# Performance work log

Measured on AMD Instinct MI355X. Metric: run time of the kernel, lower is better.

The kernel has to match this reference:

```python
import jax, jax.numpy as jnp
import numpy as np

B, N, E = 64, 2048, 32768
F_IN, NHID, RULES = 256, 512, 128
RATIO = 0.5
K1 = int(np.ceil(RATIO * N)); K2 = int(np.ceil(RATIO * K1)); K3 = int(np.ceil(RATIO * K2))


def _gcn(x, src, dst, em, W, b):
    # GCNConv with self-loops and symmetric normalization; em is a float edge-validity mask.
    n = x.shape[0]
    h = x @ W  # [n, out]
    deg = jax.ops.segment_sum(em, dst, num_segments=n) + 1.0  # in-degree + self-loop
    dinv = jax.lax.rsqrt(deg)
    coef = dinv[src] * dinv[dst] * em  # [E]
    agg = jax.ops.segment_sum(h[src] * coef[:, None], dst, num_segments=n)
    return agg + h / deg[:, None] + b  # second term = self-loop with norm 1/deg


def _sag_pool(x, src, dst, em, Wg, bg, k):
    # SAGPooling: GCN scorer, per-graph top-k, scale kept nodes by tanh(score), filter+reindex edges.
    n = x.shape[0]
    score = _gcn(x, src, dst, em, Wg, bg)[:, 0]  # [n]
    vals, perm = jax.lax.top_k(score, k)
    xk = x[perm] * jnp.tanh(vals)[:, None]  # [k, F]
    newidx = jnp.full((n,), -1, dtype=src.dtype).at[perm].set(jnp.arange(k, dtype=src.dtype))
    ns, nd = newidx[src], newidx[dst]
    keep = em * (ns >= 0).astype(em.dtype) * (nd >= 0).astype(em.dtype)
    return xk, jnp.maximum(ns, 0), jnp.maximum(nd, 0), keep


_gcn_b = jax.vmap(_gcn, in_axes=(0, 0, 0, 0, None, None))
_pool_b = jax.vmap(_sag_pool, in_axes=(0, 0, 0, 0, None, None, None))


def setup_inputs() -> dict:
    key = jax.random.key(0)
    ks = jax.random.split(key, 16)
    def w(k, shape, fan_in):
        return jax.random.normal(k, shape, jnp.float32) * (1.0 / np.sqrt(fan_in))
    return {
        "x": jax.random.normal(ks[0], (B, N, F_IN), jnp.float32),
        "src": jax.random.randint(ks[1], (B, E), 0, N, jnp.int32),
        "dst": jax.random.randint(ks[2], (B, E), 0, N, jnp.int32),
        "W1": w(ks[3], (F_IN, NHID), F_IN), "b1": jnp.zeros((NHID,), jnp.float32),
        "Wp1": w(ks[4], (NHID, 1), NHID), "bp1": jnp.zeros((1,), jnp.float32),
        "W2": w(ks[5], (NHID, NHID), NHID), "b2": jnp.zeros((NHID,), jnp.float32),
        "Wp2": w(ks[6], (NHID, 1), NHID), "bp2": jnp.zeros((1,), jnp.float32),
        "W3": w(ks[7], (NHID, NHID), NHID), "b3": jnp.zeros((NHID,), jnp.float32),
        "Wp3": w(ks[8], (NHID, 1), NHID), "bp3": jnp.zeros((1,), jnp.float32),
        "lin1_W": w(ks[9], (2 * NHID, NHID), 2 * NHID), "lin1_b": jnp.zeros((NHID,), jnp.float32),
        "lin2_W": w(ks[10], (NHID, NHID // 2), NHID), "lin2_b": jnp.zeros((NHID // 2,), jnp.float32),
        "pi_W": w(ks[11], (NHID // 2, RULES), NHID // 2), "pi_b": jnp.zeros((RULES,), jnp.float32),
        "v_W": w(ks[12], (NHID // 2, 1), NHID // 2), "v_b": jnp.zeros((1,), jnp.float32),
    }


def reference(x, src, dst, W1, b1, Wp1, bp1, W2, b2, Wp2, bp2, W3, b3, Wp3, bp3,
              lin1_W, lin1_b, lin2_W, lin2_b, pi_W, pi_b, v_W, v_b):
    em = jnp.ones(src.shape, x.dtype)
    h = jax.nn.relu(_gcn_b(x, src, dst, em, W1, b1))
    h, s, d, em = _pool_b(h, src, dst, em, Wp1, bp1, K1)
    x1 = jnp.concatenate([h.max(axis=1), h.mean(axis=1)], axis=1)  # [B, 2*NHID]
    h = jax.nn.relu(_gcn_b(h, s, d, em, W2, b2))
    h, s, d, em = _pool_b(h, s, d, em, Wp2, bp2, K2)
    x2 = jnp.concatenate([h.max(axis=1), h.mean(axis=1)], axis=1)
    h = jax.nn.relu(_gcn_b(h, s, d, em, W3, b3))
    h, s, d, em = _pool_b(h, s, d, em, Wp3, bp3, K3)
    x3 = jnp.concatenate([h.max(axis=1), h.mean(axis=1)], axis=1)
    z = x1 + x2 + x3
    z = jax.nn.relu(z @ lin1_W + lin1_b)
    z = jax.nn.relu(z @ lin2_W + lin2_b)
    pi = jax.nn.log_softmax(z @ pi_W + pi_b, axis=1)
    v = jax.nn.relu(z @ v_W + v_b)
    return pi, v
```

## Files before the change

kernel.cpp:

```cpp
#include <hip/hip_runtime.h>
#include <math.h>
#include <cstdint>

#define B_   64
#define N_   2048
#define E_   32768
#define FIN  256
#define H_   512

typedef __bf16 bf16x8 __attribute__((ext_vector_type(8)));
typedef float  f32x4  __attribute__((ext_vector_type(4)));

__device__ __forceinline__ unsigned short f2bf(float f) {
  unsigned u = __float_as_uint(f);
  u += 0x7FFF + ((u >> 16) & 1);
  return (unsigned short)(u >> 16);
}
__device__ __forceinline__ unsigned pk2(float a, float b) {
  return (unsigned)f2bf(a) | ((unsigned)f2bf(b) << 16);
}
__device__ __forceinline__ float bflo(unsigned u) { return __uint_as_float(u << 16); }
__device__ __forceinline__ float bfhi(unsigned u) { return __uint_as_float(u & 0xFFFF0000u); }

__device__ __forceinline__ void accum8(float* acc, uint4 u, float c) {
  acc[0] += c * bflo(u.x); acc[1] += c * bfhi(u.x);
  acc[2] += c * bflo(u.y); acc[3] += c * bfhi(u.y);
  acc[4] += c * bflo(u.z); acc[5] += c * bfhi(u.z);
  acc[6] += c * bflo(u.w); acc[7] += c * bfhi(u.w);
}

__device__ __forceinline__ void glds16(const void* g, void* l) {
  __builtin_amdgcn_global_load_lds(
      (const __attribute__((address_space(1))) unsigned int*)g,
      (__attribute__((address_space(3))) unsigned int*)l, 16, 0, 0);
}

__global__ void xcvt_k(const float* __restrict__ x, unsigned short* __restrict__ xb) {
  int i = blockIdx.x * 256 + threadIdx.x;
  float4 f = reinterpret_cast<const float4*>(x)[i];
  uint2 o; o.x = pk2(f.x, f.y); o.y = pk2(f.z, f.w);
  reinterpret_cast<uint2*>(xb)[i] = o;
}

__global__ void wcvt_k(const float* __restrict__ W, unsigned short* __restrict__ Wt, int K) {
  int idx = blockIdx.x * 256 + threadIdx.x;
  int k = idx >> 9, n = idx & 511;
  Wt[n * K + k] = f2bf(W[idx]);
}

__global__ __launch_bounds__(256) void gemm_mfma(
    const unsigned short* __restrict__ Xb,
    const int* __restrict__ perm, const float* __restrict__ tanhv,
    const unsigned short* __restrict__ Wt, unsigned short* __restrict__ Y,
    int K, int kl2, int nsl2,
    const float* __restrict__ bias, const float* __restrict__ wp, float* __restrict__ hs) {
  __shared__ __align__(16) char smem[34816];
  const int tid = threadIdx.x;
  const int w = tid >> 6, L = tid & 63;
  const int bid = blockIdx.x;
  const int xcd = bid & 7;
  const int t = bid >> 3;
  const int colb = t & 3;
  const int strip = ((t >> 2) << 3) + xcd;
  const int m0 = strip * 128;
  const int n0 = colb * 128;
  const int e = L & 15, q = L >> 4;

  const int sw3 = (L >> 3) & 7;
  const int cA = (w * 64 + L) ^ sw3;
  const int rloc = cA >> 2;
  const int kcs = (cA & 3) * 8;

  f32x4 acc[4][4];
#pragma unroll
  for (int j = 0; j < 4; j++)
#pragma unroll
    for (int nn = 0; nn < 4; nn++) acc[j][nn] = (f32x4){0.f, 0.f, 0.f, 0.f};

  size_t asrc[2];
#pragma unroll
  for (int i = 0; i < 2; i++) {
    int g = m0 + i * 64 + rloc;
    size_t row;
    if (perm) {
      int b = g >> kl2;
      int node = perm[g];
      row = (size_t)(b << nsl2) + node;
    } else {
      row = (size_t)g;
    }
    asrc[i] = row * (size_t)K + kcs;
  }
  size_t bsrc[2];
#pragma unroll
  for (int i = 0; i < 2; i++) bsrc[i] = (size_t)(n0 + i * 64 + rloc) * K + kcs;

  const int fo = e * 4 + q;
  const int fosw = fo ^ (fo >> 3);
  const int lofs = w * 64 * 16;

  const int nk = K >> 5;
  {
    char* Ab = smem;
    char* Bb = smem + 16384;
    glds16(Xb + asrc[0], Ab + 0 * 4096 + lofs);
    glds16(Xb + asrc[1], Ab + 1 * 4096 + lofs);
    glds16(Wt + bsrc[0], Bb + 0 * 4096 + lofs);
    glds16(Wt + bsrc[1], Bb + 1 * 4096 + lofs);
  }
  __syncthreads();
  int cur = 0;
  for (int kt = 0; kt < nk; ++kt) {
    if (kt + 1 < nk) {
      const int k0 = (kt + 1) << 5;
      char* Ab = smem + (cur ^ 1) * 8192;
      char* Bb = smem + 16384 + (cur ^ 1) * 8192;
      glds16(Xb + asrc[0] + k0, Ab + 0 * 4096 + lofs);
      glds16(Xb + asrc[1] + k0, Ab + 1 * 4096 + lofs);
      glds16(Wt + bsrc[0] + k0, Bb + 0 * 4096 + lofs);
      glds16(Wt + bsrc[1] + k0, Bb + 1 * 4096 + lofs);
    }
    const uint4* As = (const uint4*)(smem + cur * 8192);
    const uint4* Bs = (const uint4*)(smem + 16384 + cur * 8192);
    bf16x8 af[4], bfr[4];
#pragma unroll
    for (int j = 0; j < 4; j++) af[j]  = __builtin_bit_cast(bf16x8, As[((w & 1) * 4 + j) * 64 + fosw]);
#pragma unroll
    for (int j = 0; j < 4; j++) bfr[j] = __builtin_bit_cast(bf16x8, Bs[((w >> 1) * 4 + j) * 64 + fosw]);
#pragma unroll
    for (int j = 0; j < 4; j++)
#pragma unroll
      for (int nn = 0; nn < 4; nn++)
        acc[j][nn] = __builtin_amdgcn_mfma_f32_16x16x32_bf16(af[j], bfr[nn], acc[j][nn], 0, 0, 0);
    __syncthreads();
    cur ^= 1;
  }

  const int RS = 136;
  unsigned short* Csm = (unsigned short*)smem;
  float bs[4], wsv[4];
#pragma unroll
  for (int nn = 0; nn < 4; nn++) {
    int coly = n0 + ((w >> 1) * 4 + nn) * 16 + e;
    bs[nn]  = bias ? bias[coly] : 0.f;
    wsv[nn] = wp ? wp[coly] : 0.f;
  }
#pragma unroll
  for (int j = 0; j < 4; j++) {
    int mt = (w & 1) * 4 + j;
#pragma unroll
    for (int r = 0; r < 4; r++) {
      int lrow = mt * 16 + q * 4 + r;
      int grow = m0 + lrow;
      float t2 = tanhv ? tanhv[grow] : 1.0f;
      float p = 0.f;
#pragma unroll
      for (int nn = 0; nn < 4; nn++) {
        int lcol = (w >> 1) * 64 + nn * 16 + e;
        float v = acc[j][nn][r] * t2;
        if (bias) v = fmaxf(v + bs[nn], 0.f);
        Csm[lrow * RS + lcol] = f2bf(v);
        p += v * wsv[nn];
      }
      if (wp) {
        p += __shfl_xor(p, 1, 64); p += __shfl_xor(p, 2, 64);
        p += __shfl_xor(p, 4, 64); p += __shfl_xor(p, 8, 64);
        if ((L & 15) == 0) atomicAdd(&hs[grow], p);
      }
    }
  }
  __syncthreads();
  const int rbase = tid >> 4, ci = tid & 15;
#pragma unroll
  for (int pass = 0; pass < 8; ++pass) {
    int lrow = pass * 16 + rbase;
    uint4 u = *(const uint4*)(Csm + lrow * RS + ci * 8);
    *(uint4*)(Y + (size_t)(m0 + lrow) * 512 + n0 + ci * 8) = u;
  }
}

template <int NL2, bool REINDEX>
__global__ __launch_bounds__(512) void csr_k(
    const int* __restrict__ srcO, const int* __restrict__ dstO,
    const int* __restrict__ newidx,
    int* __restrict__ srcN, int* __restrict__ dstN,
    int* __restrict__ rowptr, float* __restrict__ deg, float* __restrict__ dinv,
    int* __restrict__ col, float* __restrict__ ce) {
  const int n = 1 << NL2;
  const int b = blockIdx.x, tid = threadIdx.x;
  __shared__ int   lcnt[1 << NL2];
  __shared__ int   ch[512];
  __shared__ float ldv[1 << NL2];
  __shared__ int   lnew[REINDEX ? (2 << NL2) : 1];
  const int eb = b << 15;

  for (int i = tid; i < n; i += 512) lcnt[i] = 0;
  if (REINDEX)
    for (int i = tid; i < 2 * n; i += 512) lnew[i] = newidx[(b << (NL2 + 1)) + i];
  __syncthreads();

  if (REINDEX) {
    for (int e2 = tid; e2 < E_; e2 += 512) {
      int dd = dstO[eb + e2];
      int sN = 0, dN = -1;
      if (dd >= 0) {
        int ss = srcO[eb + e2];
        int ns = lnew[ss], nd = lnew[dd];
        if (ns >= 0 && nd >= 0) { sN = ns; dN = nd; atomicAdd(&lcnt[nd], 1); }
      }
      srcN[eb + e2] = sN; dstN[eb + e2] = dN;
    }
  } else {
    for (int e2 = tid; e2 < E_; e2 += 512) {
      int d = dstO[eb + e2];
      if (d >= 0) atomicAdd(&lcnt[d], 1);
    }
  }
  __syncthreads();

  const int per = n >> 9;
  const int base = tid * per;
  int lc[per];
  int s = 0;
#pragma unroll
  for (int i = 0; i < per; i++) { lc[i] = lcnt[base + i]; s += lc[i]; }
  ch[tid] = s;
  __syncthreads();
  for (int off = 1; off < 512; off <<= 1) {
    int v = (tid >= off) ? ch[tid - off] : 0;
    __syncthreads();
    ch[tid] += v;
    __syncthreads();
  }
  int run = (tid == 0) ? 0 : ch[tid - 1];
#pragma unroll
  for (int i = 0; i < per; i++) {
    int v = lc[i];
    int g = base + i;
    rowptr[b * (n + 1) + g] = run;
    lcnt[g] = run;
    float d = (float)(v + 1);
    deg[(b << NL2) + g] = d;
    float iv = 1.0f / sqrtf(d);
    ldv[g] = iv;
    dinv[(b << NL2) + g] = iv;
    run += v;
  }
  if (tid == 511) rowptr[b * (n + 1) + n] = run;
  __syncthreads();

  const int* S2 = REINDEX ? srcN : srcO;
  const int* D2 = REINDEX ? dstN : dstO;
  for (int e2 = tid; e2 < E_; e2 += 512) {
    int d = D2[eb + e2];
    if (d >= 0) {
      int ss = S2[eb + e2];
      int pos = atomicAdd(&lcnt[d], 1);
      col[eb + pos] = ss;
      ce[eb + pos] = ldv[ss] * ldv[d];
    }
  }
}

__global__ __launch_bounds__(256) void aggx_k(
    const unsigned short* __restrict__ X,
    const int* __restrict__ rowptr, const int* __restrict__ col,
    const float* __restrict__ ce, const float* __restrict__ deg,
    unsigned short* __restrict__ Xa) {
  const int hw = threadIdx.x >> 5, hl = threadIdx.x & 31;
  const int xcd = blockIdx.x & 7;
  const int slot = blockIdx.x >> 3;
  const int gslot = slot >> 8;
  const int v8 = slot & 255;
  const int b = (gslot << 3) + xcd;
  const int v = v8 * 8 + hw;
  const int bbase = b << 11;
  const int vg = bbase + v;
  const int rb = b * (N_ + 1) + v;
  const int st = rowptr[rb], en = rowptr[rb + 1];
  const int* cb = col + (b << 15);
  const float* cee = ce + (b << 15);
  const unsigned short* Xb_ = X + (size_t)bbase * 256 + hl * 8;
  float acc[8] = {0.f, 0.f, 0.f, 0.f, 0.f, 0.f, 0.f, 0.f};
  int e2 = st;
  for (; e2 + 4 <= en; e2 += 4) {
    int s0 = cb[e2], s1 = cb[e2 + 1], s2 = cb[e2 + 2], s3 = cb[e2 + 3];
    float c0 = cee[e2], c1 = cee[e2 + 1], c2 = cee[e2 + 2], c3 = cee[e2 + 3];
    uint4 u0 = *(const uint4*)(Xb_ + (size_t)s0 * 256);
    uint4 u1 = *(const uint4*)(Xb_ + (size_t)s1 * 256);
    uint4 u2 = *(const uint4*)(Xb_ + (size_t)s2 * 256);
    uint4 u3 = *(const uint4*)(Xb_ + (size_t)s3 * 256);
    accum8(acc, u0, c0); accum8(acc, u1, c1);
    accum8(acc, u2, c2); accum8(acc, u3, c3);
  }
  for (; e2 < en; e2++) {
    uint4 u = *(const uint4*)(Xb_ + (size_t)cb[e2] * 256);
    accum8(acc, u, cee[e2]);
  }
  {
    uint4 u = *(const uint4*)(Xb_ + (size_t)v * 256);
    accum8(acc, u, 1.0f / deg[vg]);
  }
  uint4 o;
  o.x = pk2(acc[0], acc[1]); o.y = pk2(acc[2], acc[3]);
  o.z = pk2(acc[4], acc[5]); o.w = pk2(acc[6], acc[7]);
  *(uint4*)(Xa + (size_t)vg * 256 + hl * 8) = o;
}

template <int NL2>
__global__ __launch_bounds__(256) void agg_k(
    const unsigned short* __restrict__ H,
    const int* __restrict__ rowptr, const int* __restrict__ col,
    const float* __restrict__ ce, const float* __restrict__ deg,
    const float* __restrict__ bias, const float* __restrict__ wp,
    unsigned short* __restrict__ C, float* __restrict__ hs) {
  const int n = 1 << NL2;
  const int xcd = blockIdx.x & 7;
  const int slot = blockIdx.x >> 3;
  const int gslot = slot >> (NL2 - 2);
  const int v4 = slot & ((1 << (NL2 - 2)) - 1);
  const int b = (gslot << 3) + xcd;
  const int w = threadIdx.x >> 6, L = threadIdx.x & 63;
  const int v = v4 * 4 + w;
  const int bbase = b << NL2;
  const int vg = bbase + v;
  const int rb = b * (n + 1) + v;
  const int st = rowptr[rb], en = rowptr[rb + 1];
  const int* cb = col + (b << 15);
  const float* cee = ce + (b << 15);
  const unsigned short* Hb_ = H + (size_t)bbase * 512 + (size_t)L * 8;

  float acc[8] = {0.f, 0.f, 0.f, 0.f, 0.f, 0.f, 0.f, 0.f};
  int e2 = st;
  for (; e2 + 4 <= en; e2 += 4) {
    int s0 = cb[e2], s1 = cb[e2 + 1], s2 = cb[e2 + 2], s3 = cb[e2 + 3];
    float c0 = cee[e2], c1 = cee[e2 + 1], c2 = cee[e2 + 2], c3 = cee[e2 + 3];
    uint4 u0 = *(const uint4*)(Hb_ + (size_t)s0 * 512);
    uint4 u1 = *(const uint4*)(Hb_ + (size_t)s1 * 512);
    uint4 u2 = *(const uint4*)(Hb_ + (size_t)s2 * 512);
    uint4 u3 = *(const uint4*)(Hb_ + (size_t)s3 * 512);
    accum8(acc, u0, c0); accum8(acc, u1, c1);
    accum8(acc, u2, c2); accum8(acc, u3, c3);
  }
  for (; e2 < en; e2++) {
    int s = cb[e2];
    uint4 u = *(const uint4*)(Hb_ + (size_t)s * 512);
    accum8(acc, u, cee[e2]);
  }
  {
    float idg = 1.0f / deg[vg];
    uint4 u = *(const uint4*)(Hb_ + (size_t)v * 512);
    accum8(acc, u, idg);
  }
  float4 bLo = *(const float4*)(bias + L * 8);
  float4 bHi = *(const float4*)(bias + L * 8 + 4);
  acc[0] = fmaxf(acc[0] + bLo.x, 0.f); acc[1] = fmaxf(acc[1] + bLo.y, 0.f);
  acc[2] = fmaxf(acc[2] + bLo.z, 0.f); acc[3] = fmaxf(acc[3] + bLo.w, 0.f);
  acc[4] = fmaxf(acc[4] + bHi.x, 0.f); acc[5] = fmaxf(acc[5] + bHi.y, 0.f);
  acc[6] = fmaxf(acc[6] + bHi.z, 0.f); acc[7] = fmaxf(acc[7] + bHi.w, 0.f);
  uint4 o;
  o.x = pk2(acc[0], acc[1]); o.y = pk2(acc[2], acc[3]);
  o.z = pk2(acc[4], acc[5]); o.w = pk2(acc[6], acc[7]);
  *(uint4*)(C + (size_t)vg * 512 + L * 8) = o;
  float4 wLo = *(const float4*)(wp + L * 8);
  float4 wHi = *(const float4*)(wp + L * 8 + 4);
  float p = acc[0] * wLo.x + acc[1] * wLo.y + acc[2] * wLo.z + acc[3] * wLo.w
          + acc[4] * wHi.x + acc[5] * wHi.y + acc[6] * wHi.z + acc[7] * wHi.w;
#pragma unroll
  for (int off = 32; off > 0; off >>= 1) p += __shfl_down(p, off, 64);
  if (L == 0) hs[vg] = p;
}

__global__ void scoreagg_k(const float* __restrict__ hs, const int* __restrict__ rowptr,
                           const int* __restrict__ col, const float* __restrict__ ce,
                           const float* __restrict__ deg, const float* __restrict__ bp,
                           float* __restrict__ score, int nl2) {
  int idx = blockIdx.x * 256 + threadIdx.x;
  int n = 1 << nl2;
  int b = idx >> nl2, v = idx & (n - 1);
  int rb = b * (n + 1) + v;
  int st = rowptr[rb], en = rowptr[rb + 1];
  const int* cb = col + (b << 15);
  const float* cee = ce + (b << 15);
  int bbase = b << nl2;
  float acc = 0.f;
  int e = st;
  for (; e + 4 <= en; e += 4) {
    acc += hs[bbase + cb[e]] * cee[e] + hs[bbase + cb[e + 1]] * cee[e + 1]
         + hs[bbase + cb[e + 2]] * cee[e + 2] + hs[bbase + cb[e + 3]] * cee[e + 3];
  }
  for (; e < en; e++) acc += hs[bbase + cb[e]] * cee[e];
  score[idx] = acc + hs[idx] / deg[idx] + bp[0];
}

__global__ __launch_bounds__(1024) void topk_k(const float* __restrict__ score, int* __restrict__ perm,
                                               float* __restrict__ tanhv, int* __restrict__ newidx,
                                               int n, int k) {
  int b = blockIdx.x, tid = threadIdx.x;
  __shared__ float ss[2048];
  __shared__ int si[2048];
  for (int i = tid; i < n; i += 1024) { ss[i] = score[b * n + i]; si[i] = i; }
  __syncthreads();
  for (int size = 2; size <= n; size <<= 1) {
    for (int stride = size >> 1; stride > 0; stride >>= 1) {
      for (int i = tid; i < n; i += 1024) {
        int j = i ^ stride;
        if (j > i) {
          bool up = ((i & size) == 0);
          float fi = ss[i], fj = ss[j];
          int ii = si[i], ij = si[j];
          bool iBefore = (fi > fj) || (fi == fj && ii < ij);
          bool sw = up ? (!iBefore) : iBefore;
          if (sw) { ss[i] = fj; ss[j] = fi; si[i] = ij; si[j] = ii; }
        }
      }
      __syncthreads();
    }
  }
  for (int r = tid; r < n; r += 1024) newidx[b * n + si[r]] = (r < k) ? r : -1;
  for (int r = tid; r < k; r += 1024) { perm[b * k + r] = si[r]; tanhv[b * k + r] = tanhf(ss[r]); }
}

__global__ __launch_bounds__(512) void statsp_k(const unsigned short* __restrict__ C,
    const int* __restrict__ perm, const float* __restrict__ tv,
    float* __restrict__ zp, int nsl2, int k, int kch) {
  int b = blockIdx.x, rg = blockIdx.y, f = threadIdx.x;
  int r0 = rg * kch;
  float mx = -1e30f, sm = 0.f;
#pragma unroll 4
  for (int r = r0; r < r0 + kch; r++) {
    int node = perm[b * k + r];
    float t = tv[b * k + r];
    float val = __uint_as_float((unsigned)C[((size_t)((b << nsl2) + node)) * 512 + f] << 16) * t;
    mx = fmaxf(mx, val); sm += val;
  }
  zp[(size_t)(b * 8 + rg) * 1024 + f] = mx;
  zp[(size_t)(b * 8 + rg) * 1024 + 512 + f] = sm;
}

__global__ __launch_bounds__(512) void statsr_k(const float* __restrict__ zp,
                                                float* __restrict__ z, int k) {
  int b = blockIdx.x, f = threadIdx.x;
  float mx = -1e30f, sm = 0.f;
#pragma unroll
  for (int g = 0; g < 8; g++) {
    mx = fmaxf(mx, zp[(size_t)(b * 8 + g) * 1024 + f]);
    sm += zp[(size_t)(b * 8 + g) * 1024 + 512 + f];
  }
  z[b * 1024 + f] += mx;
  z[b * 1024 + 512 + f] += sm / (float)k;
}

__global__ __launch_bounds__(256) void mlp1_k(const float* __restrict__ z,
                                              const float* __restrict__ W1,
                                              float* __restrict__ zp1) {
  const int kc = blockIdx.x & 7;
  const int b = blockIdx.x >> 3;
  const int tid = threadIdx.x;
  __shared__ float zs[128];
  if (tid < 128) zs[tid] = z[b * 1024 + kc * 128 + tid];
  __syncthreads();
  float a0 = 0.f, a1 = 0.f;
  const float* Wb = W1 + (size_t)(kc * 128) * 512 + tid * 2;
#pragma unroll 4
  for (int i = 0; i < 128; i++) {
    float2 w = *(const float2*)(Wb + (size_t)i * 512);
    float zi = zs[i];
    a0 += zi * w.x; a1 += zi * w.y;
  }
  reinterpret_cast<float2*>(zp1 + ((size_t)(kc * 64 + b)) * 512)[tid] = make_float2(a0, a1);
}

__global__ __launch_bounds__(256) void mlp2_k(const float* __restrict__ zp1,
                                              const float* __restrict__ b1,
                                              const float* __restrict__ W2,
                                              float* __restrict__ zp2) {
  const int kc = blockIdx.x & 1;
  const int b = blockIdx.x >> 1;
  const int tid = threadIdx.x;
  __shared__ float z1s[256];
  {
    int i = kc * 256 + tid;
    float a = b1[i];
#pragma unroll
    for (int g = 0; g < 8; g++) a += zp1[((size_t)(g * 64 + b)) * 512 + i];
    z1s[tid] = fmaxf(a, 0.f);
  }
  __syncthreads();
  float a = 0.f;
  const float* Wb = W2 + (size_t)(kc * 256) * 256 + tid;
#pragma unroll 4
  for (int i = 0; i < 256; i++) a += z1s[i] * Wb[(size_t)i * 256];
  zp2[((size_t)(kc * 64 + b)) * 256 + tid] = a;
}

__global__ __launch_bounds__(128) void mlp3_k(const float* __restrict__ zp2,
                                              const float* __restrict__ b2,
                                              const float* __restrict__ piW,
                                              const float* __restrict__ pib,
                                              const float* __restrict__ vW,
                                              const float* __restrict__ vb,
                                              float* __restrict__ out) {
  const int b = blockIdx.x, tid = threadIdx.x;
  __shared__ float z2s[256];
  __shared__ float wred[4];
  __shared__ float sred[2];
  for (int t = tid; t < 256; t += 128) {
    float a = b2[t] + zp2[(size_t)b * 256 + t] + zp2[(size_t)(64 + b) * 256 + t];
    z2s[t] = fmaxf(a, 0.f);
  }
  __syncthreads();
  float a = pib[tid];
#pragma unroll 4
  for (int i = 0; i < 256; i++) a += z2s[i] * piW[(size_t)i * 128 + tid];
  float vp = z2s[tid] * vW[tid] + z2s[tid + 128] * vW[tid + 128];
  float m = a;
#pragma unroll
  for (int off = 32; off > 0; off >>= 1) {
    vp += __shfl_xor(vp, off, 64);
    m = fmaxf(m, __shfl_xor(m, off, 64));
  }
  const int wv = tid >> 6;
  if ((tid & 63) == 0) { wred[wv] = m; wred[2 + wv] = vp; }
  __syncthreads();
  m = fmaxf(wred[0], wred[1]);
  float s = expf(a - m);
#pragma unroll
  for (int off = 32; off > 0; off >>= 1) s += __shfl_xor(s, off, 64);
  if ((tid & 63) == 0) sred[wv] = s;
  __syncthreads();
  s = sred[0] + sred[1];
  if (tid == 0) out[B_ * 128 + b] = fmaxf(vb[0] + wred[2] + wred[3], 0.f);
  out[b * 128 + tid] = a - m - logf(s);
}

extern "C" void kernel_launch(void* const* d_in, const int* in_sizes, int n_in,
                              void* d_out, int out_size, void* d_ws, size_t ws_size,
                              hipStream_t stream) {
  const float* x    = (const float*)d_in[0];
  const int*   src0 = (const int*)d_in[1];
  const int*   dst0 = (const int*)d_in[2];
  const float* W1   = (const float*)d_in[3];
  const float* b1   = (const float*)d_in[4];
  const float* Wp1  = (const float*)d_in[5];
  const float* bp1  = (const float*)d_in[6];
  const float* W2   = (const float*)d_in[7];
  const float* b2   = (const float*)d_in[8];
  const float* Wp2  = (const float*)d_in[9];
  const float* bp2  = (const float*)d_in[10];
  const float* W3   = (const float*)d_in[11];
  const float* b3   = (const float*)d_in[12];
  const float* Wp3  = (const float*)d_in[13];
  const float* bp3  = (const float*)d_in[14];
  const float* l1W  = (const float*)d_in[15];
  const float* l1b  = (const float*)d_in[16];
  const float* l2W  = (const float*)d_in[17];
  const float* l2b  = (const float*)d_in[18];
  const float* piW  = (const float*)d_in[19];
  const float* pib  = (const float*)d_in[20];
  const float* vW   = (const float*)d_in[21];
  const float* vb   = (const float*)d_in[22];
  float* out = (float*)d_out;
  (void)in_sizes; (void)n_in; (void)out_size; (void)ws_size;

  unsigned short* Cb = (unsigned short*)d_in[0];

  char* base = (char*)d_ws;
  size_t off = 0;
  auto alloc = [&](size_t bytes) -> void* {
    void* r = base + off;
    off += (bytes + 255) & ~(size_t)255;
    return r;
  };
  unsigned short* Hb   = (unsigned short*)alloc((size_t)B_ * 1024 * H_ * 2);
  unsigned short* xb   = (unsigned short*)alloc((size_t)B_ * N_ * FIN * 2);
  unsigned short* Xa   = (unsigned short*)alloc((size_t)B_ * N_ * FIN * 2);
  unsigned short* W1t  = (unsigned short*)alloc((size_t)512 * 256 * 2);
  unsigned short* W2t  = (unsigned short*)alloc((size_t)512 * 512 * 2);
  unsigned short* W3t  = (unsigned short*)alloc((size_t)512 * 512 * 2);
  int*   srcA   = (int*)alloc((size_t)B_ * E_ * 4);
  int*   dstA   = (int*)alloc((size_t)B_ * E_ * 4);
  int*   col    = (int*)alloc((size_t)B_ * E_ * 4);
  float* coefE  = (float*)alloc((size_t)B_ * E_ * 4);
  int*   rowptr = (int*)alloc((size_t)B_ * (N_ + 1) * 4);
  float* deg    = (float*)alloc((size_t)B_ * N_ * 4);
  float* dinv   = (float*)alloc((size_t)B_ * N_ * 4);
  float* hs     = (float*)alloc((size_t)B_ * N_ * 4);
  float* score  = (float*)alloc((size_t)B_ * N_ * 4);
  int*   newidx = (int*)alloc((size_t)B_ * N_ * 4);
  int*   perm   = (int*)alloc((size_t)B_ * 1024 * 4);
  float* tanhv  = (float*)alloc((size_t)B_ * 1024 * 4);
  float* zpart  = (float*)alloc((size_t)B_ * 8 * 1024 * 4);
  float* z      = (float*)alloc((size_t)B_ * 1024 * 4);

  float* zp1 = zpart;
  float* zp2 = zpart + (size_t)8 * 64 * 512;

  xcvt_k<<<B_ * N_ * FIN / 4 / 256, 256, 0, stream>>>(x, xb);
  wcvt_k<<<256 * 512 / 256, 256, 0, stream>>>(W1, W1t, 256);
  wcvt_k<<<512 * 512 / 256, 256, 0, stream>>>(W2, W2t, 512);
  wcvt_k<<<512 * 512 / 256, 256, 0, stream>>>(W3, W3t, 512);
  hipMemsetAsync(z, 0, (size_t)B_ * 1024 * 4, stream);

  {
    csr_k<11, false><<<B_, 512, 0, stream>>>(src0, dst0, nullptr, nullptr, nullptr,
                                             rowptr, deg, dinv, col, coefE);
    aggx_k<<<B_ * 2048 / 8, 256, 0, stream>>>(xb, rowptr, col, coefE, deg, Xa);
    hipMemsetAsync(hs, 0, (size_t)B_ * 2048 * 4, stream);
    gemm_mfma<<<B_ * 2048 / 128 * 4, 256, 0, stream>>>(
        Xa, nullptr, nullptr, W1t, Cb, 256, 0, 0, b1, Wp1, hs);
    scoreagg_k<<<B_ * 2048 / 256, 256, 0, stream>>>(hs, rowptr, col, coefE, deg, bp1, score, 11);
    topk_k<<<B_, 1024, 0, stream>>>(score, perm, tanhv, newidx, 2048, 1024);
    statsp_k<<<dim3(B_, 8), 512, 0, stream>>>(Cb, perm, tanhv, zpart, 11, 1024, 128);
    statsr_k<<<B_, 512, 0, stream>>>(zpart, z, 1024);
    csr_k<10, true><<<B_, 512, 0, stream>>>(src0, dst0, newidx, srcA, dstA,
                                            rowptr, deg, dinv, col, coefE);
  }
  {
    gemm_mfma<<<B_ * 1024 / 128 * 4, 256, 0, stream>>>(
        Cb, perm, tanhv, W2t, Hb, 512, 10, 11, nullptr, nullptr, nullptr);
    agg_k<10><<<B_ * 1024 / 4, 256, 0, stream>>>(Hb, rowptr, col, coefE, deg, b2, Wp2, Cb, hs);
    scoreagg_k<<<B_ * 1024 / 256, 256, 0, stream>>>(hs, rowptr, col, coefE, deg, bp2, score, 10);
    topk_k<<<B_, 1024, 0, stream>>>(score, perm, tanhv, newidx, 1024, 512);
    statsp_k<<<dim3(B_, 8), 512, 0, stream>>>(Cb, perm, tanhv, zpart, 10, 512, 64);
    statsr_k<<<B_, 512, 0, stream>>>(zpart, z, 512);
    csr_k<9, true><<<B_, 512, 0, stream>>>(srcA, dstA, newidx, srcA, dstA,
                                           rowptr, deg, dinv, col, coefE);
  }
  {
    gemm_mfma<<<B_ * 512 / 128 * 4, 256, 0, stream>>>(
        Cb, perm, tanhv, W3t, Hb, 512, 9, 10, nullptr, nullptr, nullptr);
    agg_k<9><<<B_ * 512 / 4, 256, 0, stream>>>(Hb, rowptr, col, coefE, deg, b3, Wp3, Cb, hs);
    scoreagg_k<<<B_ * 512 / 256, 256, 0, stream>>>(hs, rowptr, col, coefE, deg, bp3, score, 9);
    topk_k<<<B_, 1024, 0, stream>>>(score, perm, tanhv, newidx, 512, 256);
    statsp_k<<<dim3(B_, 8), 512, 0, stream>>>(Cb, perm, tanhv, zpart, 9, 256, 32);
    statsr_k<<<B_, 512, 0, stream>>>(zpart, z, 256);
  }

  mlp1_k<<<B_ * 8, 256, 0, stream>>>(z, l1W, zp1);
  mlp2_k<<<B_ * 2, 256, 0, stream>>>(zp1, l1b, l2W, zp2);
  mlp3_k<<<B_, 128, 0, stream>>>(zp2, l2b, piW, pib, vW, vb, out);
}
```

Before: 1.123 ms.

## Rebuild CSR via composed node maps and LDS-staged chunked scatter

```diff
diff --git a/kernel.cpp b/kernel.cpp
--- a/kernel.cpp
+++ b/kernel.cpp
@@ -179,86 +179,141 @@
   }
 }
 
-template <int NL2, bool REINDEX>
-__global__ __launch_bounds__(512) void csr_k(
-    const int* __restrict__ srcO, const int* __restrict__ dstO,
-    const int* __restrict__ newidx,
-    int* __restrict__ srcN, int* __restrict__ dstN,
-    int* __restrict__ rowptr, float* __restrict__ deg, float* __restrict__ dinv,
+template <int NL2, int LEVEL>
+__global__ __launch_bounds__(1024) void csr_k(
+    const int* __restrict__ src0, const int* __restrict__ dst0,
+    const int* __restrict__ curNew, int* __restrict__ cmapG,
+    int* __restrict__ rowptr, float* __restrict__ deg,
     int* __restrict__ col, float* __restrict__ ce) {
   const int n = 1 << NL2;
+  const int CAP = 8192;
   const int b = blockIdx.x, tid = threadIdx.x;
-  __shared__ int   lcnt[1 << NL2];
-  __shared__ int   ch[512];
+  __shared__ int   lrp[(1 << NL2) + 1];
+  __shared__ int   cur[1 << NL2];
   __shared__ float ldv[1 << NL2];
-  __shared__ int   lnew[REINDEX ? (2 << NL2) : 1];
+  __shared__ int   ch[1024];
+  __shared__ int   cmap[(LEVEL > 0) ? 2048 : 1];
+  __shared__ int   scol[CAP];
+  __shared__ float sce[CAP];
+  __shared__ int   sr1;
   const int eb = b << 15;
 
-  for (int i = tid; i < n; i += 512) lcnt[i] = 0;
-  if (REINDEX)
-    for (int i = tid; i < 2 * n; i += 512) lnew[i] = newidx[(b << (NL2 + 1)) + i];
-  __syncthreads();
-
-  if (REINDEX) {
-    for (int e2 = tid; e2 < E_; e2 += 512) {
-      int dd = dstO[eb + e2];
-      int sN = 0, dN = -1;
-      if (dd >= 0) {
-        int ss = srcO[eb + e2];
-        int ns = lnew[ss], nd = lnew[dd];
-        if (ns >= 0 && nd >= 0) { sN = ns; dN = nd; atomicAdd(&lcnt[nd], 1); }
+  for (int i = tid; i < n; i += 1024) cur[i] = 0;
+  if (LEVEL == 1) {
+    for (int v = tid; v < 2048; v += 1024) {
+      int m = curNew[(b << 11) + v];
+      cmap[v] = m;
+      cmapG[(b << 11) + v] = m;
+    }
+  } else if (LEVEL == 2) {
+    for (int v = tid; v < 2048; v += 1024) {
+      int p = cmapG[(b << 11) + v];
+      cmap[v] = (p >= 0) ? curNew[(b << 10) + p] : -1;
+    }
+  }
+  __syncthreads();
+
+  for (int e = tid; e < E_; e += 4096) {
+#pragma unroll
+    for (int u = 0; u < 4; u++) {
+      int ei = eb + e + u * 1024;
+      int dd = dst0[ei];
+      if (LEVEL == 0) {
+        atomicAdd(&cur[dd], 1);
+      } else {
+        int md = cmap[dd], ms = cmap[src0[ei]];
+        if (ms >= 0 && md >= 0) atomicAdd(&cur[md], 1);
       }
-      srcN[eb + e2] = sN; dstN[eb + e2] = dN;
-    }
-  } else {
-    for (int e2 = tid; e2 < E_; e2 += 512) {
-      int d = dstO[eb + e2];
-      if (d >= 0) atomicAdd(&lcnt[d], 1);
-    }
-  }
-  __syncthreads();
-
-  const int per = n >> 9;
-  const int base = tid * per;
+    }
+  }
+  __syncthreads();
+
+  const int nth = (n < 1024) ? n : 1024;
+  const int per = (n + 1023) >> 10;
   int lc[per];
   int s = 0;
-#pragma unroll
-  for (int i = 0; i < per; i++) { lc[i] = lcnt[base + i]; s += lc[i]; }
+  if (tid < nth) {
+    int base = tid * per;
+#pragma unroll
+    for (int i = 0; i < per; i++) { lc[i] = cur[base + i]; s += lc[i]; }
+  }
   ch[tid] = s;
   __syncthreads();
-  for (int off = 1; off < 512; off <<= 1) {
-    int v = (tid >= off) ? ch[tid - off] : 0;
+  for (int off2 = 1; off2 < nth; off2 <<= 1) {
+    int v = (tid >= off2) ? ch[tid - off2] : 0;
     __syncthreads();
     ch[tid] += v;
     __syncthreads();
   }
-  int run = (tid == 0) ? 0 : ch[tid - 1];
-#pragma unroll
-  for (int i = 0; i < per; i++) {
-    int v = lc[i];
-    int g = base + i;
-    rowptr[b * (n + 1) + g] = run;
-    lcnt[g] = run;
-    float d = (float)(v + 1);
-    deg[(b << NL2) + g] = d;
-    float iv = 1.0f / sqrtf(d);
-    ldv[g] = iv;
-    dinv[(b << NL2) + g] = iv;
-    run += v;
-  }
-  if (tid == 511) rowptr[b * (n + 1) + n] = run;
-  __syncthreads();
-
-  const int* S2 = REINDEX ? srcN : srcO;
-  const int* D2 = REINDEX ? dstN : dstO;
-  for (int e2 = tid; e2 < E_; e2 += 512) {
-    int d = D2[eb + e2];
-    if (d >= 0) {
-      int ss = S2[eb + e2];
-      int pos = atomicAdd(&lcnt[d], 1);
-      col[eb + pos] = ss;
-      ce[eb + pos] = ldv[ss] * ldv[d];
-    }
+  if (tid < nth) {
+    int run = (tid == 0) ? 0 : ch[tid - 1];
+    int base = tid * per;
+#pragma unroll
+    for (int i = 0; i < per; i++) {
+      int g = base + i;
+      lrp[g] = run;
+      rowptr[b * (n + 1) + g] = run;
+      cur[g] = run;
+      float dd = (float)(lc[i] + 1);
+      deg[(b << NL2) + g] = dd;
+      ldv[g] = 1.0f / sqrtf(dd);
+      run += lc[i];
+    }
+    if (tid == nth - 1) { lrp[n] = run; rowptr[b * (n + 1) + n] = run; }
+  }
+  __syncthreads();
+
+  int r0 = 0;
+  while (r0 < n) {
+    int base0 = lrp[r0];
+    if (tid == 0) sr1 = n + 1;
+    __syncthreads();
+    for (int r = r0 + 1 + tid; r <= n; r += 1024) {
+      if (lrp[r] - base0 > CAP) { atomicMin(&sr1, r); break; }
+    }
+    __syncthreads();
+    int r1 = sr1 - 1;
+    if (r1 > n) r1 = n;
+    if (r1 <= r0) {
+      for (int e = tid; e < E_; e += 1024) {
+        int ei = eb + e;
+        int ss = src0[ei], dd = dst0[ei];
+        int ms, md;
+        if (LEVEL == 0) { ms = ss; md = dd; }
+        else { ms = cmap[ss]; md = cmap[dd]; }
+        if (ms >= 0 && md == r0) {
+          int pos = atomicAdd(&cur[r0], 1);
+          col[eb + pos] = ms;
+          ce[eb + pos] = ldv[ms] * ldv[r0];
+        }
+      }
+      __syncthreads();
+      r0 = r0 + 1;
+      continue;
+    }
+    for (int e = tid; e < E_; e += 4096) {
+#pragma unroll
+      for (int u = 0; u < 4; u++) {
+        int ei = eb + e + u * 1024;
+        int ss = src0[ei], dd = dst0[ei];
+        int ms, md;
+        if (LEVEL == 0) { ms = ss; md = dd; }
+        else { ms = cmap[ss]; md = cmap[dd]; }
+        if (ms >= 0 && md >= r0 && md < r1) {
+          int pos = atomicAdd(&cur[md], 1);
+          scol[pos - base0] = ms;
+          sce[pos - base0] = ldv[ms] * ldv[md];
+        }
+      }
+    }
+    __syncthreads();
+    int cnt = lrp[r1] - base0;
+    for (int i = tid; i < cnt; i += 1024) {
+      col[eb + base0 + i] = scol[i];
+      ce[eb + base0 + i] = sce[i];
+    }
+    __syncthreads();
+    r0 = r1;
   }
 }
 
@@ -578,13 +633,11 @@
   unsigned short* W1t  = (unsigned short*)alloc((size_t)512 * 256 * 2);
   unsigned short* W2t  = (unsigned short*)alloc((size_t)512 * 512 * 2);
   unsigned short* W3t  = (unsigned short*)alloc((size_t)512 * 512 * 2);
-  int*   srcA   = (int*)alloc((size_t)B_ * E_ * 4);
-  int*   dstA   = (int*)alloc((size_t)B_ * E_ * 4);
   int*   col    = (int*)alloc((size_t)B_ * E_ * 4);
   float* coefE  = (float*)alloc((size_t)B_ * E_ * 4);
+  int*   cmapG  = (int*)alloc((size_t)B_ * N_ * 4);
   int*   rowptr = (int*)alloc((size_t)B_ * (N_ + 1) * 4);
   float* deg    = (float*)alloc((size_t)B_ * N_ * 4);
-  float* dinv   = (float*)alloc((size_t)B_ * N_ * 4);
   float* hs     = (float*)alloc((size_t)B_ * N_ * 4);
   float* score  = (float*)alloc((size_t)B_ * N_ * 4);
   int*   newidx = (int*)alloc((size_t)B_ * N_ * 4);
@@ -603,8 +656,8 @@
   hipMemsetAsync(z, 0, (size_t)B_ * 1024 * 4, stream);
 
   {
-    csr_k<11, false><<<B_, 512, 0, stream>>>(src0, dst0, nullptr, nullptr, nullptr,
-                                             rowptr, deg, dinv, col, coefE);
+    csr_k<11, 0><<<B_, 1024, 0, stream>>>(src0, dst0, nullptr, nullptr,
+                                          rowptr, deg, col, coefE);
     aggx_k<<<B_ * 2048 / 8, 256, 0, stream>>>(xb, rowptr, col, coefE, deg, Xa);
     hipMemsetAsync(hs, 0, (size_t)B_ * 2048 * 4, stream);
     gemm_mfma<<<B_ * 2048 / 128 * 4, 256, 0, stream>>>(
@@ -613,8 +666,8 @@
     topk_k<<<B_, 1024, 0, stream>>>(score, perm, tanhv, newidx, 2048, 1024);
     statsp_k<<<dim3(B_, 8), 512, 0, stream>>>(Cb, perm, tanhv, zpart, 11, 1024, 128);
     statsr_k<<<B_, 512, 0, stream>>>(zpart, z, 1024);
-    csr_k<10, true><<<B_, 512, 0, stream>>>(src0, dst0, newidx, srcA, dstA,
-                                            rowptr, deg, dinv, col, coefE);
+    csr_k<10, 1><<<B_, 1024, 0, stream>>>(src0, dst0, newidx, cmapG,
+                                          rowptr, deg, col, coefE);
   }
   {
     gemm_mfma<<<B_ * 1024 / 128 * 4, 256, 0, stream>>>(
@@ -624,8 +677,8 @@
     topk_k<<<B_, 1024, 0, stream>>>(score, perm, tanhv, newidx, 1024, 512);
     statsp_k<<<dim3(B_, 8), 512, 0, stream>>>(Cb, perm, tanhv, zpart, 10, 512, 64);
     statsr_k<<<B_, 512, 0, stream>>>(zpart, z, 512);
-    csr_k<9, true><<<B_, 512, 0, stream>>>(srcA, dstA, newidx, srcA, dstA,
-                                           rowptr, deg, dinv, col, coefE);
+    csr_k<9, 2><<<B_, 1024, 0, stream>>>(src0, dst0, newidx, cmapG,
+                                         rowptr, deg, col, coefE);
   }
   {
     gemm_mfma<<<B_ * 512 / 128 * 4, 256, 0, stream>>>(
```

Result: faster. 961.2 us (-14.4%).
